# Kernel optimization log

Measured on AMD Instinct MI355X. Metric: run time of the kernel, lower is better.

## Reference

```python
import jax, jax.numpy as jnp
import numpy as np

D_MODEL = 256
D_INNER = 512   # expand=2
D_STATE = 16
D_CONV = 4
DT_RANK = 16    # ceil(d_model/16)
EPS = 1e-5


def _ln(x, g, b):
    m = x.mean(-1, keepdims=True)
    v = jnp.mean((x - m) ** 2, -1, keepdims=True)
    return (x - m) * jax.lax.rsqrt(v + EPS) * g + b


def _mamba(x, W_in, conv_w, conv_b, W_x, W_dt, b_dt, A_log, Dp, W_out):
    B, N, _ = x.shape
    xz = x @ W_in.T                               # [B,N,2*Di]
    xs, z = jnp.split(xz, 2, axis=-1)
    # depthwise causal conv1d, kernel D_CONV, left pad D_CONV-1
    xp = jnp.pad(xs, ((0, 0), (D_CONV - 1, 0), (0, 0)))
    xc = sum(xp[:, k:k + N, :] * conv_w[:, k] for k in range(D_CONV)) + conv_b
    xc = jax.nn.silu(xc)                          # [B,N,Di]
    dbl = xc @ W_x.T                              # [B,N,dt_rank+2*S]
    dt, Bm, Cm = jnp.split(dbl, [DT_RANK, DT_RANK + D_STATE], axis=-1)
    dt = jax.nn.softplus(dt @ W_dt.T + b_dt)      # [B,N,Di]
    A = -jnp.exp(A_log)                           # [Di,S]
    dA = jnp.exp(dt[..., None] * A)               # [B,N,Di,S]
    dBx = dt[..., None] * Bm[:, :, None, :] * xc[..., None]

    def step(h, inp):
        dA_t, dBx_t, c_t = inp                    # [B,Di,S],[B,Di,S],[B,S]
        h = dA_t * h + dBx_t
        y = jnp.einsum('bds,bs->bd', h, c_t)
        return h, y

    h0 = jnp.zeros((B, D_INNER, D_STATE), xs.dtype)
    _, ys = jax.lax.scan(step, h0, (dA.swapaxes(0, 1), dBx.swapaxes(0, 1), Cm.swapaxes(0, 1)))
    y = ys.swapaxes(0, 1) + Dp * xc
    y = y * jax.nn.silu(z)
    return y @ W_out.T                            # [B,N,d_model]


def setup_inputs() -> dict:
    key = jax.random.key(0)
    ks = jax.random.split(key, 24)
    g = lambda k, s, sc=0.02: jax.random.normal(k, s, jnp.float32) * sc
    inp = {}
    inp['input_states'] = jax.random.normal(ks[0], (1, 8192, D_MODEL), jnp.float32)
    inp['position_states'] = jax.random.normal(ks[1], (1, 8192, D_MODEL), jnp.float32)
    inp['W_in'] = g(ks[2], (2 * D_INNER, D_MODEL))
    inp['conv_w'] = g(ks[3], (D_INNER, D_CONV), 0.2)
    inp['conv_b'] = jnp.zeros((D_INNER,), jnp.float32)
    inp['W_x'] = g(ks[4], (DT_RANK + 2 * D_STATE, D_INNER))
    inp['W_dt'] = g(ks[5], (D_INNER, DT_RANK), 0.1)
    inp['b_dt'] = g(ks[6], (D_INNER,), 0.1)
    # S4D-real init: A_log = log(1..d_state) broadcast over channels
    inp['A_log'] = jnp.log(jnp.broadcast_to(jnp.arange(1, D_STATE + 1, dtype=jnp.float32), (D_INNER, D_STATE)))
    inp['Dp'] = jnp.ones((D_INNER,), jnp.float32)
    inp['W_out'] = g(ks[7], (D_MODEL, D_INNER))
    inp['W_lin'] = g(ks[8], (D_MODEL, D_MODEL))
    inp['b_lin'] = jnp.zeros((D_MODEL,), jnp.float32)
    inp['ln1_g'] = jnp.ones((D_MODEL,), jnp.float32)
    inp['ln1_b'] = jnp.zeros((D_MODEL,), jnp.float32)
    inp['W_exp'] = g(ks[9], (2 * D_MODEL, D_MODEL))
    inp['b_exp'] = jnp.zeros((2 * D_MODEL,), jnp.float32)
    inp['W_sq'] = g(ks[10], (D_MODEL, 2 * D_MODEL))
    inp['b_sq'] = jnp.zeros((D_MODEL,), jnp.float32)
    inp['ln2_g'] = jnp.ones((D_MODEL,), jnp.float32)
    inp['ln2_b'] = jnp.zeros((D_MODEL,), jnp.float32)
    return inp


def reference(input_states, position_states, W_in, conv_w, conv_b, W_x, W_dt, b_dt,
              A_log, Dp, W_out, W_lin, b_lin, ln1_g, ln1_b, W_exp, b_exp, W_sq, b_sq,
              ln2_g, ln2_b):
    h = _mamba(input_states, W_in, conv_w, conv_b, W_x, W_dt, b_dt, A_log, Dp, W_out)
    h = h @ W_lin.T + b_lin
    h = _ln(h + input_states, ln1_g, ln1_b)
    ff = jax.nn.relu(h @ W_exp.T + b_exp) @ W_sq.T + b_sq
    out = _ln(h + ff, ln2_g, ln2_b)
    # RPEMamba returns (hidden, input_states) as (states, attention_scores)
    return out, input_states
```

## Files before the change

kernel.cpp:

```cpp
#include <hip/hip_runtime.h>
#include <stdint.h>

#define NT 8192
#define DM 256
#define DI 512
#define DS 16
#define DR 16
#define NCH 512
#define LCH 16
#define NSUP 32
#define CPS 16

typedef __bf16 bf16_t;
typedef bf16_t bf16x8 __attribute__((ext_vector_type(8)));
typedef float f32x4 __attribute__((ext_vector_type(4)));

__device__ __forceinline__ unsigned short f2b(float f) {
    union { float f; unsigned int i; } v; v.f = f;
    unsigned int r = v.i + 0x7fffu + ((v.i >> 16) & 1u);
    return (unsigned short)(r >> 16);
}
__device__ __forceinline__ float b2f(unsigned short u) {
    union { unsigned int i; float f; } v; v.i = ((unsigned int)u) << 16; return v.f;
}
__device__ __forceinline__ bf16x8 ld_frag_lds(const unsigned short* p) {
    union { uint4 u; bf16x8 b; } v;
    v.u = *(const uint4*)p;
    return v.b;
}
__device__ __forceinline__ void async16(const unsigned short* g, unsigned short* l) {
    __builtin_amdgcn_global_load_lds(
        (const __attribute__((address_space(1))) unsigned int*)g,
        (__attribute__((address_space(3))) unsigned int*)l, 16, 0, 0);
}
__device__ __forceinline__ float fast_softplus(float x) {
    return x > 20.f ? x : __logf(1.f + __expf(x));
}
__device__ __forceinline__ float silu(float x) {
    return x / (1.f + __expf(-x));
}

struct PrepArgs {
    const float* src[6];
    unsigned short* dst[6];
    int cnt[6];
    int cvt_blocks;
    const float* W_dt;
    const float* W_x;
    unsigned short* wbig;
};
__global__ __launch_bounds__(256) void prep(PrepArgs a) {
    int blk = blockIdx.x;
    if (blk < a.cvt_blocks) {
        int i = blk * 256 + threadIdx.x;
        #pragma unroll
        for (int s = 0; s < 6; s++) {
            if (i < a.cnt[s]) {
                unsigned short v = f2b(a.src[s][i]);
                if (s == 2) {
                    int k = i >> 9, j = i & 511;
                    a.dst[s][j * 256 + k] = v;
                } else {
                    a.dst[s][i] = v;
                }
                return;
            }
            i -= a.cnt[s];
        }
    } else if (blk < a.cvt_blocks + 1024) {
        int i = (blk - a.cvt_blocks) * 256 + threadIdx.x;
        int d = i >> 9, k = i & 511;
        float acc = 0.f;
        #pragma unroll
        for (int j = 0; j < 16; j++) acc += a.W_dt[d * 16 + j] * a.W_x[j * 512 + k];
        a.wbig[d * 512 + k] = f2b(acc);
    } else {
        int i = (blk - a.cvt_blocks - 1024) * 256 + threadIdx.x;
        int j = i >> 9, k = i & 511;
        a.wbig[(512 + j) * 512 + k] = f2b(a.W_x[(16 + j) * 512 + k]);
    }
}

template<int BM, int BN, int FLAGS>
__global__ __launch_bounds__(256) void gemm_lds(
    const unsigned short* __restrict__ A, const unsigned short* __restrict__ B,
    int M, int N, int K,
    const float* __restrict__ bias, const float* __restrict__ resid,
    float* __restrict__ Cf, unsigned short* __restrict__ Cb,
    float* __restrict__ Cf2)
{
    constexpr int MI = BM / 32;
    constexpr int NJ = BN / 32;
    __shared__ unsigned short sA[BM * 64];
    __shared__ unsigned short sB[BN * 64];
    const int tid = threadIdx.x;
    const int m0 = blockIdx.x * BM;
    const int n0 = blockIdx.y * BN;
    const int wave = tid >> 6, lane = tid & 63;
    const int wm = (wave & 1) * (BM / 2);
    const int wn = (wave >> 1) * (BN / 2);
    const int qm = lane >> 4, rm = lane & 15;

    f32x4 acc[MI][NJ];
    #pragma unroll
    for (int i = 0; i < MI; i++)
        #pragma unroll
        for (int j = 0; j < NJ; j++)
            #pragma unroll
            for (int r = 0; r < 4; r++) acc[i][j][r] = 0.f;

    const int sr = tid >> 3;
    const int sc = (tid & 7) * 8;

    for (int k0 = 0; k0 < K; k0 += 64) {
        __syncthreads();
        #pragma unroll
        for (int j = 0; j < BM / 32; j++) {
            int r = sr + j * 32;
            async16(A + (size_t)(m0 + r) * K + k0 + sc, &sA[r * 64 + sc]);
        }
        #pragma unroll
        for (int j = 0; j < BN / 32; j++) {
            int r = sr + j * 32;
            if (n0 + r < N)
                async16(B + (size_t)(n0 + r) * K + k0 + sc, &sB[r * 64 + sc]);
        }
        __syncthreads();
        #pragma unroll
        for (int ks = 0; ks < 64; ks += 32) {
            bf16x8 af[MI], bfr[NJ];
            #pragma unroll
            for (int i = 0; i < MI; i++)
                af[i] = ld_frag_lds(&sA[(wm + i * 16 + rm) * 64 + ks + qm * 8]);
            #pragma unroll
            for (int j = 0; j < NJ; j++)
                bfr[j] = ld_frag_lds(&sB[(wn + j * 16 + rm) * 64 + ks + qm * 8]);
            #pragma unroll
            for (int i = 0; i < MI; i++)
                #pragma unroll
                for (int j = 0; j < NJ; j++)
                    acc[i][j] = __builtin_amdgcn_mfma_f32_16x16x32_bf16(
                        af[i], bfr[j], acc[i][j], 0, 0, 0);
        }
    }

    #pragma unroll
    for (int i = 0; i < MI; i++) {
        int mrow = m0 + wm + i * 16 + qm * 4;
        #pragma unroll
        for (int j = 0; j < NJ; j++) {
            int ncol = n0 + wn + j * 16 + rm;
            if (ncol < N) {
                #pragma unroll
                for (int r = 0; r < 4; r++) {
                    float v = acc[i][j][r];
                    int mm = mrow + r;
                    if constexpr (FLAGS & 32) {
                        if (ncol < 512) {
                            v = fast_softplus(v + bias[ncol]);
                            Cf[(size_t)mm * 512 + ncol] = v;
                        } else {
                            Cf2[(size_t)mm * 32 + (ncol - 512)] = v;
                        }
                    } else {
                        if constexpr (FLAGS & 1) v += bias[ncol];
                        if constexpr (FLAGS & 4) v += resid[(size_t)mm * N + ncol];
                        if constexpr (FLAGS & 2) v = v > 0.f ? v : 0.f;
                        if constexpr (FLAGS & 8) Cf[(size_t)mm * N + ncol] = v;
                        if constexpr (FLAGS & 16) Cb[(size_t)mm * N + ncol] = f2b(v);
                    }
                }
            }
        }
    }
}

__global__ __launch_bounds__(256) void conv_silu_b(
    const unsigned short* __restrict__ xz, const float* __restrict__ cw,
    const float* __restrict__ cb, unsigned short* __restrict__ xcb)
{
    int idx = blockIdx.x * 256 + threadIdx.x;
    int d = idx & (DI - 1), t = idx >> 9;
    float v = cb[d];
    #pragma unroll
    for (int k = 0; k < 4; k++) {
        int tt = t - 3 + k;
        if (tt >= 0) v += b2f(xz[(size_t)tt * 1024 + d]) * cw[d * 4 + k];
    }
    xcb[idx] = f2b(silu(v));
}

__global__ __launch_bounds__(256) void scan1(
    const unsigned short* __restrict__ xcb, const float* __restrict__ dtf,
    const float* __restrict__ dblf, const float* __restrict__ A_log,
    unsigned short* __restrict__ Acb, unsigned short* __restrict__ Bcb)
{
    __shared__ float sBC[LCH * 32];
    const int tid = threadIdx.x;
    const int d = blockIdx.x * 128 + (tid >> 1);
    const int sd = tid & 1;
    const int c = blockIdx.y;
    const int t0 = c * LCH;
    if (tid < 128)
        ((float4*)sBC)[tid] = ((const float4*)(dblf + (size_t)t0 * 32))[tid];
    __syncthreads();
    float A2[8], h[8];
    #pragma unroll
    for (int s = 0; s < 8; s++) {
        A2[s] = -__expf(A_log[d * 16 + sd * 8 + s]) * 1.44269504f;
        h[s] = 0.f;
    }
    float sumdt = 0.f;
    #pragma unroll 4
    for (int t = 0; t < LCH; t++) {
        float dtv = dtf[(size_t)(t0 + t) * DI + d];
        float xcv = b2f(xcb[(size_t)(t0 + t) * DI + d]);
        float dtx = dtv * xcv;
        sumdt += dtv;
        const float4 b0 = *(const float4*)&sBC[t * 32 + sd * 8];
        const float4 b1 = *(const float4*)&sBC[t * 32 + sd * 8 + 4];
        float bb[8] = {b0.x, b0.y, b0.z, b0.w, b1.x, b1.y, b1.z, b1.w};
        #pragma unroll
        for (int s = 0; s < 8; s++)
            h[s] = exp2f(dtv * A2[s]) * h[s] + dtx * bb[s];
    }
    #pragma unroll
    for (int s = 0; s < 8; s++) {
        size_t off = ((size_t)c * DS + sd * 8 + s) * DI + d;
        Acb[off] = f2b(exp2f(sumdt * A2[s]));
        Bcb[off] = f2b(h[s]);
    }
}

__global__ __launch_bounds__(256) void scan2a(
    const unsigned short* __restrict__ Acb, const unsigned short* __restrict__ Bcb,
    unsigned short* __restrict__ Apb, unsigned short* __restrict__ Hlb,
    float* __restrict__ Es, float* __restrict__ Ds)
{
    int p = blockIdx.x * 256 + threadIdx.x;
    int j = blockIdx.y;
    float h = 0.f, P = 1.f;
    for (int cc = 0; cc < CPS; cc++) {
        size_t off = (size_t)(j * CPS + cc) * 8192 + p;
        Hlb[off] = f2b(h); Apb[off] = f2b(P);
        h = b2f(Acb[off]) * h + b2f(Bcb[off]);
        P *= b2f(Acb[off]);
    }
    Es[(size_t)j * 8192 + p] = h;
    Ds[(size_t)j * 8192 + p] = P;
}

__global__ __launch_bounds__(256) void scan2b(
    const float* __restrict__ Es, const float* __restrict__ Ds,
    float* __restrict__ Ss)
{
    int p = blockIdx.x * 256 + threadIdx.x;
    float S = 0.f;
    for (int j = 0; j < NSUP; j++) {
        Ss[(size_t)j * 8192 + p] = S;
        S = Ds[(size_t)j * 8192 + p] * S + Es[(size_t)j * 8192 + p];
    }
}

__global__ __launch_bounds__(256) void scan3(
    const unsigned short* __restrict__ xcb, const float* __restrict__ dtf,
    const float* __restrict__ dblf, const unsigned short* __restrict__ xzb,
    const float* __restrict__ A_log, const float* __restrict__ Dpp,
    const unsigned short* __restrict__ Apb, const unsigned short* __restrict__ Hlb,
    const float* __restrict__ Ss, unsigned short* __restrict__ ygb)
{
    __shared__ float sBC[LCH * 32];
    const int tid = threadIdx.x;
    const int d = blockIdx.x * 128 + (tid >> 1);
    const int sd = tid & 1;
    const int c = blockIdx.y;
    const int jsup = c / CPS;
    const int t0 = c * LCH;
    if (tid < 128)
        ((float4*)sBC)[tid] = ((const float4*)(dblf + (size_t)t0 * 32))[tid];
    __syncthreads();
    float A2[8], h[8];
    #pragma unroll
    for (int s = 0; s < 8; s++) {
        A2[s] = -__expf(A_log[d * 16 + sd * 8 + s]) * 1.44269504f;
        size_t off = (size_t)c * 8192 + (sd * 8 + s) * DI + d;
        h[s] = b2f(Apb[off]) * Ss[(size_t)jsup * 8192 + (sd * 8 + s) * DI + d]
             + b2f(Hlb[off]);
    }
    const float dpv = Dpp[d];
    #pragma unroll 4
    for (int t = 0; t < LCH; t++) {
        float dtv = dtf[(size_t)(t0 + t) * DI + d];
        float xcv = b2f(xcb[(size_t)(t0 + t) * DI + d]);
        float zv  = b2f(xzb[(size_t)(t0 + t) * 1024 + DI + d]);
        float dtx = dtv * xcv;
        const float4 b0 = *(const float4*)&sBC[t * 32 + sd * 8];
        const float4 b1 = *(const float4*)&sBC[t * 32 + sd * 8 + 4];
        const float4 c0 = *(const float4*)&sBC[t * 32 + 16 + sd * 8];
        const float4 c1 = *(const float4*)&sBC[t * 32 + 16 + sd * 8 + 4];
        float bb[8] = {b0.x, b0.y, b0.z, b0.w, b1.x, b1.y, b1.z, b1.w};
        float cc[8] = {c0.x, c0.y, c0.z, c0.w, c1.x, c1.y, c1.z, c1.w};
        float y = 0.f;
        #pragma unroll
        for (int s = 0; s < 8; s++) {
            h[s] = exp2f(dtv * A2[s]) * h[s] + dtx * bb[s];
            y += h[s] * cc[s];
        }
        y += __shfl_xor(y, 1, 64);
        if (!sd)
            ygb[(size_t)(t0 + t) * DI + d] = f2b((y + dpv * xcv) * silu(zv));
    }
}

__global__ __launch_bounds__(256) void lnorm(
    const float* __restrict__ X, const float* __restrict__ X2,
    const float* __restrict__ g, const float* __restrict__ b,
    float* __restrict__ outf, unsigned short* __restrict__ outb,
    const float* __restrict__ csrc, float* __restrict__ cdst)
{
    int wave = threadIdx.x >> 6, lane = threadIdx.x & 63;
    int row = blockIdx.x * 4 + wave;
    const float* x = X + (size_t)row * DM;
    float v[4];
    #pragma unroll
    for (int i = 0; i < 4; i++) {
        int col = lane + i * 64;
        v[i] = x[col];
        if (X2) v[i] += X2[(size_t)row * DM + col];
    }
    if (cdst) {
        #pragma unroll
        for (int i = 0; i < 4; i++) {
            int col = lane + i * 64;
            cdst[(size_t)row * DM + col] = csrc[(size_t)row * DM + col];
        }
    }
    float s = v[0] + v[1] + v[2] + v[3];
    float s2 = v[0]*v[0] + v[1]*v[1] + v[2]*v[2] + v[3]*v[3];
    #pragma unroll
    for (int m = 1; m < 64; m <<= 1) {
        s  += __shfl_xor(s, m, 64);
        s2 += __shfl_xor(s2, m, 64);
    }
    float mean = s * (1.f / DM);
    float var = s2 * (1.f / DM) - mean * mean;
    float inv = rsqrtf(var + 1e-5f);
    #pragma unroll
    for (int i = 0; i < 4; i++) {
        int col = lane + i * 64;
        float o = (v[i] - mean) * inv * g[col] + b[col];
        if (outf) outf[(size_t)row * DM + col] = o;
        if (outb) outb[(size_t)row * DM + col] = f2b(o);
    }
}

static constexpr size_t OFF_XZB   = 0;
static constexpr size_t OFF_XCB   = 16777216;
static constexpr size_t OFF_DTF   = 25165824;
static constexpr size_t OFF_DBLF  = 41943040;
static constexpr size_t OFF_ACB   = 42991616;
static constexpr size_t OFF_BCB   = 51380224;
static constexpr size_t OFF_APB   = 59768832;
static constexpr size_t OFF_HLB   = 68157440;
static constexpr size_t OFF_ES    = 76546048;
static constexpr size_t OFF_DS2   = 77594624;
static constexpr size_t OFF_SS    = 78643200;
static constexpr size_t OFF_YGB   = 79691776;
static constexpr size_t OFF_XB    = 88080384;
static constexpr size_t OFF_WINB  = 92274688;
static constexpr size_t OFF_WOUTT = 92798976;
static constexpr size_t OFF_WLINB = 93061120;
static constexpr size_t OFF_WEXPB = 93192192;
static constexpr size_t OFF_WSQB  = 93454336;
static constexpr size_t OFF_WCOMB = 93716480;
static constexpr size_t OFF_WBIG  = 93978624;
static constexpr size_t OFF_H2    = 94535680;
static constexpr size_t OFF_HLN   = 102924288;
static constexpr size_t OFF_HLNB  = 111312896;
static constexpr size_t OFF_FF1B  = 115507200;
static constexpr size_t OFF_FF2   = 123895808;

extern "C" void kernel_launch(void* const* d_in, const int* in_sizes, int n_in,
                              void* d_out, int out_size, void* d_ws, size_t ws_size,
                              hipStream_t stream)
{
    const float* x      = (const float*)d_in[0];
    const float* W_in   = (const float*)d_in[2];
    const float* conv_w = (const float*)d_in[3];
    const float* conv_b = (const float*)d_in[4];
    const float* W_x    = (const float*)d_in[5];
    const float* W_dt   = (const float*)d_in[6];
    const float* b_dt   = (const float*)d_in[7];
    const float* A_log  = (const float*)d_in[8];
    const float* Dp     = (const float*)d_in[9];
    const float* W_out  = (const float*)d_in[10];
    const float* W_lin  = (const float*)d_in[11];
    const float* b_lin  = (const float*)d_in[12];
    const float* ln1_g  = (const float*)d_in[13];
    const float* ln1_b  = (const float*)d_in[14];
    const float* W_exp  = (const float*)d_in[15];
    const float* b_exp  = (const float*)d_in[16];
    const float* W_sq   = (const float*)d_in[17];
    const float* b_sq   = (const float*)d_in[18];
    const float* ln2_g  = (const float*)d_in[19];
    const float* ln2_b  = (const float*)d_in[20];

    char* ws = (char*)d_ws;
    unsigned short* xzb = (unsigned short*)(ws + OFF_XZB);
    unsigned short* xcb = (unsigned short*)(ws + OFF_XCB);
    float* dtf  = (float*)(ws + OFF_DTF);
    float* dblf = (float*)(ws + OFF_DBLF);
    unsigned short* Acb = (unsigned short*)(ws + OFF_ACB);
    unsigned short* Bcb = (unsigned short*)(ws + OFF_BCB);
    unsigned short* Apb = (unsigned short*)(ws + OFF_APB);
    unsigned short* Hlb = (unsigned short*)(ws + OFF_HLB);
    float* Es   = (float*)(ws + OFF_ES);
    float* Ds   = (float*)(ws + OFF_DS2);
    float* Ss   = (float*)(ws + OFF_SS);
    unsigned short* ygb   = (unsigned short*)(ws + OFF_YGB);
    unsigned short* xb    = (unsigned short*)(ws + OFF_XB);
    unsigned short* winb  = (unsigned short*)(ws + OFF_WINB);
    unsigned short* woutT = (unsigned short*)(ws + OFF_WOUTT);
    unsigned short* wlinb = (unsigned short*)(ws + OFF_WLINB);
    unsigned short* wexpb = (unsigned short*)(ws + OFF_WEXPB);
    unsigned short* wsqb  = (unsigned short*)(ws + OFF_WSQB);
    unsigned short* wcomb = (unsigned short*)(ws + OFF_WCOMB);
    unsigned short* wbig  = (unsigned short*)(ws + OFF_WBIG);
    float* h2   = (float*)(ws + OFF_H2);
    float* hln  = (float*)(ws + OFF_HLN);
    unsigned short* hlnb  = (unsigned short*)(ws + OFF_HLNB);
    unsigned short* ff1b  = (unsigned short*)(ws + OFF_FF1B);
    float* ff2  = (float*)(ws + OFF_FF2);
    float* outp = (float*)d_out;

    PrepArgs pa;
    pa.src[0] = x;     pa.dst[0] = xb;    pa.cnt[0] = NT * DM;
    pa.src[1] = W_in;  pa.dst[1] = winb;  pa.cnt[1] = 1024 * DM;
    pa.src[2] = W_out; pa.dst[2] = woutT; pa.cnt[2] = DM * DI;
    pa.src[3] = W_lin; pa.dst[3] = wlinb; pa.cnt[3] = DM * DM;
    pa.src[4] = W_exp; pa.dst[4] = wexpb; pa.cnt[4] = DI * DM;
    pa.src[5] = W_sq;  pa.dst[5] = wsqb;  pa.cnt[5] = DM * DI;
    pa.cvt_blocks = (2097152 + 262144 + 131072 + 65536 + 131072 + 131072) / 256;
    pa.W_dt = W_dt; pa.W_x = W_x; pa.wbig = wbig;
    prep<<<pa.cvt_blocks + 1024 + 64, 256, 0, stream>>>(pa);

    gemm_lds<64,64,16><<<dim3(4, 8), 256, 0, stream>>>(wlinb, woutT, DM, DI, DM,
        nullptr, nullptr, nullptr, wcomb, nullptr);
    gemm_lds<128,128,16><<<dim3(64, 8), 256, 0, stream>>>(xb, winb, NT, 1024, DM,
        nullptr, nullptr, nullptr, xzb, nullptr);
    conv_silu_b<<<NT * DI / 256, 256, 0, stream>>>(xzb, conv_w, conv_b, xcb);
    gemm_lds<64,64,32><<<dim3(128, 9), 256, 0, stream>>>(xcb, wbig, NT, 544, DI,
        b_dt, nullptr, dtf, nullptr, dblf);
    scan1<<<dim3(4, NCH), 256, 0, stream>>>(xcb, dtf, dblf, A_log, Acb, Bcb);
    scan2a<<<dim3(32, NSUP), 256, 0, stream>>>(Acb, Bcb, Apb, Hlb, Es, Ds);
    scan2b<<<32, 256, 0, stream>>>(Es, Ds, Ss);
    scan3<<<dim3(4, NCH), 256, 0, stream>>>(xcb, dtf, dblf, xzb, A_log, Dp,
                                            Apb, Hlb, Ss, ygb);
    gemm_lds<64,64,1|4|8><<<dim3(128, 4), 256, 0, stream>>>(ygb, wcomb, NT, DM, DI,
        b_lin, x, h2, nullptr, nullptr);
    lnorm<<<NT / 4, 256, 0, stream>>>(h2, nullptr, ln1_g, ln1_b, hln, hlnb,
                                      nullptr, nullptr);
    gemm_lds<64,128,1|2|16><<<dim3(128, 4), 256, 0, stream>>>(hlnb, wexpb, NT, DI, DM,
        b_exp, nullptr, nullptr, ff1b, nullptr);
    gemm_lds<64,64,1|8><<<dim3(128, 4), 256, 0, stream>>>(ff1b, wsqb, NT, DM, DI,
        b_sq, nullptr, ff2, nullptr, nullptr);
    lnorm<<<NT / 4, 256, 0, stream>>>(hln, ff2, ln2_g, ln2_b, outp, nullptr,
                                      x, outp + (size_t)NT * DM);
}
```

Before: 279.1 us.

## Fuse LayerNorm into output GEMMs and fold W_lin·W_out into prep kernel

Adds a gemm_ln kernel in which each block computes full 256-wide rows (a 32-row tile), then applies bias, the residual add and LayerNorm in the epilogue. This replaces the two gemm+lnorm pairs and removes the fp32 h2/ff2 intermediates and their round trips through global memory. The W_lin·W_out combined-weight GEMM moves into the prep kernel as a naive fp32 dot loop, saving one launch. Risks: only 256 blocks per fused GEMM, which lowers parallelism, and a slow 256-iteration serial loop in prep for 512 blocks.

```diff
diff --git a/kernel.cpp b/kernel.cpp
--- a/kernel.cpp
+++ b/kernel.cpp
@@ -41,30 +41,24 @@
 }
 
 struct PrepArgs {
-    const float* src[6];
-    unsigned short* dst[6];
-    int cnt[6];
+    const float* src[4];
+    unsigned short* dst[4];
+    int cnt[4];
     int cvt_blocks;
     const float* W_dt;
     const float* W_x;
+    const float* W_lin;
+    const float* W_out;
     unsigned short* wbig;
+    unsigned short* wcomb;
 };
 __global__ __launch_bounds__(256) void prep(PrepArgs a) {
     int blk = blockIdx.x;
     if (blk < a.cvt_blocks) {
         int i = blk * 256 + threadIdx.x;
         #pragma unroll
-        for (int s = 0; s < 6; s++) {
-            if (i < a.cnt[s]) {
-                unsigned short v = f2b(a.src[s][i]);
-                if (s == 2) {
-                    int k = i >> 9, j = i & 511;
-                    a.dst[s][j * 256 + k] = v;
-                } else {
-                    a.dst[s][i] = v;
-                }
-                return;
-            }
+        for (int s = 0; s < 4; s++) {
+            if (i < a.cnt[s]) { a.dst[s][i] = f2b(a.src[s][i]); return; }
             i -= a.cnt[s];
         }
     } else if (blk < a.cvt_blocks + 1024) {
@@ -74,10 +68,16 @@
         #pragma unroll
         for (int j = 0; j < 16; j++) acc += a.W_dt[d * 16 + j] * a.W_x[j * 512 + k];
         a.wbig[d * 512 + k] = f2b(acc);
-    } else {
+    } else if (blk < a.cvt_blocks + 1024 + 64) {
         int i = (blk - a.cvt_blocks - 1024) * 256 + threadIdx.x;
         int j = i >> 9, k = i & 511;
         a.wbig[(512 + j) * 512 + k] = f2b(a.W_x[(16 + j) * 512 + k]);
+    } else {
+        int i = (blk - a.cvt_blocks - 1024 - 64) * 256 + threadIdx.x;
+        int r = i >> 9, j = i & 511;
+        float acc = 0.f;
+        for (int k = 0; k < 256; k++) acc += a.W_lin[r * 256 + k] * a.W_out[k * 512 + j];
+        a.wcomb[r * 512 + j] = f2b(acc);
     }
 }
 
@@ -85,7 +85,7 @@
 __global__ __launch_bounds__(256) void gemm_lds(
     const unsigned short* __restrict__ A, const unsigned short* __restrict__ B,
     int M, int N, int K,
-    const float* __restrict__ bias, const float* __restrict__ resid,
+    const float* __restrict__ bias,
     float* __restrict__ Cf, unsigned short* __restrict__ Cb,
     float* __restrict__ Cf2)
 {
@@ -164,7 +164,6 @@
                         }
                     } else {
                         if constexpr (FLAGS & 1) v += bias[ncol];
-                        if constexpr (FLAGS & 4) v += resid[(size_t)mm * N + ncol];
                         if constexpr (FLAGS & 2) v = v > 0.f ? v : 0.f;
                         if constexpr (FLAGS & 8) Cf[(size_t)mm * N + ncol] = v;
                         if constexpr (FLAGS & 16) Cb[(size_t)mm * N + ncol] = f2b(v);
@@ -173,6 +172,115 @@
             }
         }
     }
+}
+
+__global__ __launch_bounds__(256) void gemm_ln(
+    const unsigned short* __restrict__ A, const unsigned short* __restrict__ B,
+    int K,
+    const float* __restrict__ bias, const float* __restrict__ add,
+    const float* __restrict__ g, const float* __restrict__ bv,
+    float* __restrict__ outf, unsigned short* __restrict__ outb,
+    const float* __restrict__ csrc, float* __restrict__ cdst)
+{
+    __shared__ unsigned short sA[32 * 64];
+    __shared__ unsigned short sB[256 * 64];
+    __shared__ float sSum[4][32];
+    __shared__ float sSum2[4][32];
+    const int tid = threadIdx.x;
+    const int m0 = blockIdx.x * 32;
+    const int wave = tid >> 6, lane = tid & 63;
+    const int wn = wave * 64;
+    const int qm = lane >> 4, rm = lane & 15;
+
+    f32x4 acc[2][4];
+    #pragma unroll
+    for (int i = 0; i < 2; i++)
+        #pragma unroll
+        for (int j = 0; j < 4; j++)
+            #pragma unroll
+            for (int r = 0; r < 4; r++) acc[i][j][r] = 0.f;
+
+    const int sr = tid >> 3;
+    const int sc = (tid & 7) * 8;
+
+    for (int k0 = 0; k0 < K; k0 += 64) {
+        __syncthreads();
+        async16(A + (size_t)(m0 + sr) * K + k0 + sc, &sA[sr * 64 + sc]);
+        #pragma unroll
+        for (int j = 0; j < 8; j++) {
+            int r = sr + j * 32;
+            async16(B + (size_t)r * K + k0 + sc, &sB[r * 64 + sc]);
+        }
+        __syncthreads();
+        #pragma unroll
+        for (int ks = 0; ks < 64; ks += 32) {
+            bf16x8 af[2], bfr[4];
+            #pragma unroll
+            for (int i = 0; i < 2; i++)
+                af[i] = ld_frag_lds(&sA[(i * 16 + rm) * 64 + ks + qm * 8]);
+            #pragma unroll
+            for (int j = 0; j < 4; j++)
+                bfr[j] = ld_frag_lds(&sB[(wn + j * 16 + rm) * 64 + ks + qm * 8]);
+            #pragma unroll
+            for (int i = 0; i < 2; i++)
+                #pragma unroll
+                for (int j = 0; j < 4; j++)
+                    acc[i][j] = __builtin_amdgcn_mfma_f32_16x16x32_bf16(
+                        af[i], bfr[j], acc[i][j], 0, 0, 0);
+        }
+    }
+
+    float v[2][4][4];
+    #pragma unroll
+    for (int i = 0; i < 2; i++)
+        #pragma unroll
+        for (int j = 0; j < 4; j++) {
+            int col = wn + j * 16 + rm;
+            #pragma unroll
+            for (int r = 0; r < 4; r++) {
+                int row = m0 + i * 16 + qm * 4 + r;
+                v[i][j][r] = acc[i][j][r] + bias[col] + add[(size_t)row * DM + col];
+            }
+        }
+    #pragma unroll
+    for (int i = 0; i < 2; i++)
+        #pragma unroll
+        for (int r = 0; r < 4; r++) {
+            float s  = v[i][0][r] + v[i][1][r] + v[i][2][r] + v[i][3][r];
+            float s2 = v[i][0][r]*v[i][0][r] + v[i][1][r]*v[i][1][r]
+                     + v[i][2][r]*v[i][2][r] + v[i][3][r]*v[i][3][r];
+            #pragma unroll
+            for (int m = 1; m < 16; m <<= 1) {
+                s  += __shfl_xor(s, m, 64);
+                s2 += __shfl_xor(s2, m, 64);
+            }
+            if (rm == 0) {
+                int rl = i * 16 + qm * 4 + r;
+                sSum[wave][rl] = s;
+                sSum2[wave][rl] = s2;
+            }
+        }
+    __syncthreads();
+    #pragma unroll
+    for (int i = 0; i < 2; i++)
+        #pragma unroll
+        for (int r = 0; r < 4; r++) {
+            int rl = i * 16 + qm * 4 + r;
+            int row = m0 + rl;
+            float tot  = sSum[0][rl] + sSum[1][rl] + sSum[2][rl] + sSum[3][rl];
+            float tot2 = sSum2[0][rl] + sSum2[1][rl] + sSum2[2][rl] + sSum2[3][rl];
+            float mean = tot * (1.f / DM);
+            float var  = tot2 * (1.f / DM) - mean * mean;
+            float inv  = rsqrtf(var + 1e-5f);
+            #pragma unroll
+            for (int j = 0; j < 4; j++) {
+                int col = wn + j * 16 + rm;
+                float o = (v[i][j][r] - mean) * inv * g[col] + bv[col];
+                outf[(size_t)row * DM + col] = o;
+                if (outb) outb[(size_t)row * DM + col] = f2b(o);
+                if (cdst) cdst[(size_t)row * DM + col] = csrc[(size_t)row * DM + col];
+            }
+        }
 }
 
 __global__ __launch_bounds__(256) void conv_silu_b(
@@ -312,48 +420,6 @@
     }
 }
 
-__global__ __launch_bounds__(256) void lnorm(
-    const float* __restrict__ X, const float* __restrict__ X2,
-    const float* __restrict__ g, const float* __restrict__ b,
-    float* __restrict__ outf, unsigned short* __restrict__ outb,
-    const float* __restrict__ csrc, float* __restrict__ cdst)
-{
-    int wave = threadIdx.x >> 6, lane = threadIdx.x & 63;
-    int row = blockIdx.x * 4 + wave;
-    const float* x = X + (size_t)row * DM;
-    float v[4];
-    #pragma unroll
-    for (int i = 0; i < 4; i++) {
-        int col = lane + i * 64;
-        v[i] = x[col];
-        if (X2) v[i] += X2[(size_t)row * DM + col];
-    }
-    if (cdst) {
-        #pragma unroll
-        for (int i = 0; i < 4; i++) {
-            int col = lane + i * 64;
-            cdst[(size_t)row * DM + col] = csrc[(size_t)row * DM + col];
-        }
-    }
-    float s = v[0] + v[1] + v[2] + v[3];
-    float s2 = v[0]*v[0] + v[1]*v[1] + v[2]*v[2] + v[3]*v[3];
-    #pragma unroll
-    for (int m = 1; m < 64; m <<= 1) {
-        s  += __shfl_xor(s, m, 64);
-        s2 += __shfl_xor(s2, m, 64);
-    }
-    float mean = s * (1.f / DM);
-    float var = s2 * (1.f / DM) - mean * mean;
-    float inv = rsqrtf(var + 1e-5f);
-    #pragma unroll
-    for (int i = 0; i < 4; i++) {
-        int col = lane + i * 64;
-        float o = (v[i] - mean) * inv * g[col] + b[col];
-        if (outf) outf[(size_t)row * DM + col] = o;
-        if (outb) outb[(size_t)row * DM + col] = f2b(o);
-    }
-}
-
 static constexpr size_t OFF_XZB   = 0;
 static constexpr size_t OFF_XCB   = 16777216;
 static constexpr size_t OFF_DTF   = 25165824;
@@ -368,17 +434,13 @@
 static constexpr size_t OFF_YGB   = 79691776;
 static constexpr size_t OFF_XB    = 88080384;
 static constexpr size_t OFF_WINB  = 92274688;
-static constexpr size_t OFF_WOUTT = 92798976;
-static constexpr size_t OFF_WLINB = 93061120;
-static constexpr size_t OFF_WEXPB = 93192192;
-static constexpr size_t OFF_WSQB  = 93454336;
-static constexpr size_t OFF_WCOMB = 93716480;
-static constexpr size_t OFF_WBIG  = 93978624;
-static constexpr size_t OFF_H2    = 94535680;
-static constexpr size_t OFF_HLN   = 102924288;
-static constexpr size_t OFF_HLNB  = 111312896;
-static constexpr size_t OFF_FF1B  = 115507200;
-static constexpr size_t OFF_FF2   = 123895808;
+static constexpr size_t OFF_WEXPB = 92798976;
+static constexpr size_t OFF_WSQB  = 93061120;
+static constexpr size_t OFF_WCOMB = 93323264;
+static constexpr size_t OFF_WBIG  = 93585408;
+static constexpr size_t OFF_HLN   = 94142464;
+static constexpr size_t OFF_HLNB  = 102531072;
+static constexpr size_t OFF_FF1B  = 106725376;
 
 extern "C" void kernel_launch(void* const* d_in, const int* in_sizes, int n_in,
                               void* d_out, int out_size, void* d_ws, size_t ws_size,
@@ -420,50 +482,40 @@
     unsigned short* ygb   = (unsigned short*)(ws + OFF_YGB);
     unsigned short* xb    = (unsigned short*)(ws + OFF_XB);
     unsigned short* winb  = (unsigned short*)(ws + OFF_WINB);
-    unsigned short* woutT = (unsigned short*)(ws + OFF_WOUTT);
-    unsigned short* wlinb = (unsigned short*)(ws + OFF_WLINB);
     unsigned short* wexpb = (unsigned short*)(ws + OFF_WEXPB);
     unsigned short* wsqb  = (unsigned short*)(ws + OFF_WSQB);
     unsigned short* wcomb = (unsigned short*)(ws + OFF_WCOMB);
     unsigned short* wbig  = (unsigned short*)(ws + OFF_WBIG);
-    float* h2   = (float*)(ws + OFF_H2);
     float* hln  = (float*)(ws + OFF_HLN);
     unsigned short* hlnb  = (unsigned short*)(ws + OFF_HLNB);
     unsigned short* ff1b  = (unsigned short*)(ws + OFF_FF1B);
-    float* ff2  = (float*)(ws + OFF_FF2);
     float* outp = (float*)d_out;
 
     PrepArgs pa;
     pa.src[0] = x;     pa.dst[0] = xb;    pa.cnt[0] = NT * DM;
     pa.src[1] = W_in;  pa.dst[1] = winb;  pa.cnt[1] = 1024 * DM;
-    pa.src[2] = W_out; pa.dst[2] = woutT; pa.cnt[2] = DM * DI;
-    pa.src[3] = W_lin; pa.dst[3] = wlinb; pa.cnt[3] = DM * DM;
-    pa.src[4] = W_exp; pa.dst[4] = wexpb; pa.cnt[4] = DI * DM;
-    pa.src[5] = W_sq;  pa.dst[5] = wsqb;  pa.cnt[5] = DM * DI;
-    pa.cvt_blocks = (2097152 + 262144 + 131072 + 65536 + 131072 + 131072) / 256;
-    pa.W_dt = W_dt; pa.W_x = W_x; pa.wbig = wbig;
-    prep<<<pa.cvt_blocks + 1024 + 64, 256, 0, stream>>>(pa);
-
-    gemm_lds<64,64,16><<<dim3(4, 8), 256, 0, stream>>>(wlinb, woutT, DM, DI, DM,
-        nullptr, nullptr, nullptr, wcomb, nullptr);
+    pa.src[2] = W_exp; pa.dst[2] = wexpb; pa.cnt[2] = DI * DM;
+    pa.src[3] = W_sq;  pa.dst[3] = wsqb;  pa.cnt[3] = DM * DI;
+    pa.cvt_blocks = (2097152 + 262144 + 131072 + 131072) / 256;
+    pa.W_dt = W_dt; pa.W_x = W_x; pa.W_lin = W_lin; pa.W_out = W_out;
+    pa.wbig = wbig; pa.wcomb = wcomb;
+    prep<<<pa.cvt_blocks + 1024 + 64 + 512, 256, 0, stream>>>(pa);
+
     gemm_lds<128,128,16><<<dim3(64, 8), 256, 0, stream>>>(xb, winb, NT, 1024, DM,
-        nullptr, nullptr, nullptr, xzb, nullptr);
+        nullptr, nullptr, xzb, nullptr);
     conv_silu_b<<<NT * DI / 256, 256, 0, stream>>>(xzb, conv_w, conv_b, xcb);
     gemm_lds<64,64,32><<<dim3(128, 9), 256, 0, stream>>>(xcb, wbig, NT, 544, DI,
-        b_dt, nullptr, dtf, nullptr, dblf);
+        b_dt, dtf, nullptr, dblf);
     scan1<<<dim3(4, NCH), 256, 0, stream>>>(xcb, dtf, dblf, A_log, Acb, Bcb);
     scan2a<<<dim3(32, NSUP), 256, 0, stream>>>(Acb, Bcb, Apb, Hlb, Es, Ds);
     scan2b<<<32, 256, 0, stream>>>(Es, Ds, Ss);
     scan3<<<dim3(4, NCH), 256, 0, stream>>>(xcb, dtf, dblf, xzb, A_log, Dp,
                                             Apb, Hlb, Ss, ygb);
-    gemm_lds<64,64,1|4|8><<<dim3(128, 4), 256, 0, stream>>>(ygb, wcomb, NT, DM, DI,
-        b_lin, x, h2, nullptr, nullptr);
-    lnorm<<<NT / 4, 256, 0, stream>>>(h2, nullptr, ln1_g, ln1_b, hln, hlnb,
-                                      nullptr, nullptr);
+    gemm_ln<<<NT / 32, 256, 0, stream>>>(ygb, wcomb, DI, b_lin, x,
+                                         ln1_g, ln1_b, hln, hlnb, nullptr, nullptr);
     gemm_lds<64,128,1|2|16><<<dim3(128, 4), 256, 0, stream>>>(hlnb, wexpb, NT, DI, DM,
-        b_exp, nullptr, nullptr, ff1b, nullptr);
-    gemm_lds<64,64,1|8><<<dim3(128, 4), 256, 0, stream>>>(ff1b, wsqb, NT, DM, DI,
-        b_sq, nullptr, ff2, nullptr, nullptr);
-    lnorm<<<NT / 4, 256, 0, stream>>>(hln, ff2, ln2_g, ln2_b, outp, nullptr,
-                                      x, outp + (size_t)NT * DM);
-}
+        b_exp, nullptr, ff1b, nullptr);
+    gemm_ln<<<NT / 32, 256, 0, stream>>>(ff1b, wsqb, DI, b_sq, hln,
+                                         ln2_g, ln2_b, outp, nullptr,
+                                         x, outp + (size_t)NT * DM);
+}
```

Measured after the change: 294.2 us. 1.05x slower.

## Store dt in bf16, split scan state across 4 lanes, fold W_lin*W_out into prep

Applied to the files above, without the earlier changes.

The dt projection output is now written as bf16 instead of fp32, which halves the traffic that scan1 and scan3 spend reading it. The scan kernels now give each channel 4 lanes with 4 states each instead of 2 lanes with 8, doubling the grid for more parallelism and fewer registers per thread. The combined W_lin·W_out weight is now computed directly in the prep kernel with a naive fp32 loop, removing two conversions and a separate GEMM launch. The risks are lower precision in dt and an extra shuffle stage for the y reduction.

```diff
diff --git a/kernel.cpp b/kernel.cpp
--- a/kernel.cpp
+++ b/kernel.cpp
@@ -41,30 +41,24 @@
 }
 
 struct PrepArgs {
-    const float* src[6];
-    unsigned short* dst[6];
-    int cnt[6];
+    const float* src[4];
+    unsigned short* dst[4];
+    int cnt[4];
     int cvt_blocks;
     const float* W_dt;
     const float* W_x;
+    const float* W_lin;
+    const float* W_out;
     unsigned short* wbig;
+    unsigned short* wcomb;
 };
 __global__ __launch_bounds__(256) void prep(PrepArgs a) {
     int blk = blockIdx.x;
     if (blk < a.cvt_blocks) {
         int i = blk * 256 + threadIdx.x;
         #pragma unroll
-        for (int s = 0; s < 6; s++) {
-            if (i < a.cnt[s]) {
-                unsigned short v = f2b(a.src[s][i]);
-                if (s == 2) {
-                    int k = i >> 9, j = i & 511;
-                    a.dst[s][j * 256 + k] = v;
-                } else {
-                    a.dst[s][i] = v;
-                }
-                return;
-            }
+        for (int s = 0; s < 4; s++) {
+            if (i < a.cnt[s]) { a.dst[s][i] = f2b(a.src[s][i]); return; }
             i -= a.cnt[s];
         }
     } else if (blk < a.cvt_blocks + 1024) {
@@ -74,10 +68,16 @@
         #pragma unroll
         for (int j = 0; j < 16; j++) acc += a.W_dt[d * 16 + j] * a.W_x[j * 512 + k];
         a.wbig[d * 512 + k] = f2b(acc);
-    } else {
+    } else if (blk < a.cvt_blocks + 1024 + 64) {
         int i = (blk - a.cvt_blocks - 1024) * 256 + threadIdx.x;
         int j = i >> 9, k = i & 511;
         a.wbig[(512 + j) * 512 + k] = f2b(a.W_x[(16 + j) * 512 + k]);
+    } else {
+        int i = (blk - a.cvt_blocks - 1024 - 64) * 256 + threadIdx.x;
+        int r = i >> 9, j = i & 511;
+        float acc = 0.f;
+        for (int k = 0; k < 256; k++) acc += a.W_lin[r * 256 + k] * a.W_out[k * 512 + j];
+        a.wcomb[r * 512 + j] = f2b(acc);
     }
 }
 
@@ -158,7 +158,7 @@
                     if constexpr (FLAGS & 32) {
                         if (ncol < 512) {
                             v = fast_softplus(v + bias[ncol]);
-                            Cf[(size_t)mm * 512 + ncol] = v;
+                            Cb[(size_t)mm * 512 + ncol] = f2b(v);
                         } else {
                             Cf2[(size_t)mm * 32 + (ncol - 512)] = v;
                         }
@@ -191,42 +191,41 @@
 }
 
 __global__ __launch_bounds__(256) void scan1(
-    const unsigned short* __restrict__ xcb, const float* __restrict__ dtf,
+    const unsigned short* __restrict__ xcb, const unsigned short* __restrict__ dtb,
     const float* __restrict__ dblf, const float* __restrict__ A_log,
     unsigned short* __restrict__ Acb, unsigned short* __restrict__ Bcb)
 {
     __shared__ float sBC[LCH * 32];
     const int tid = threadIdx.x;
-    const int d = blockIdx.x * 128 + (tid >> 1);
-    const int sd = tid & 1;
+    const int d = blockIdx.x * 64 + (tid >> 2);
+    const int sd = tid & 3;
     const int c = blockIdx.y;
     const int t0 = c * LCH;
     if (tid < 128)
         ((float4*)sBC)[tid] = ((const float4*)(dblf + (size_t)t0 * 32))[tid];
     __syncthreads();
-    float A2[8], h[8];
-    #pragma unroll
-    for (int s = 0; s < 8; s++) {
-        A2[s] = -__expf(A_log[d * 16 + sd * 8 + s]) * 1.44269504f;
+    float A2[4], h[4];
+    #pragma unroll
+    for (int s = 0; s < 4; s++) {
+        A2[s] = -__expf(A_log[d * 16 + sd * 4 + s]) * 1.44269504f;
         h[s] = 0.f;
     }
     float sumdt = 0.f;
     #pragma unroll 4
     for (int t = 0; t < LCH; t++) {
-        float dtv = dtf[(size_t)(t0 + t) * DI + d];
+        float dtv = b2f(dtb[(size_t)(t0 + t) * DI + d]);
         float xcv = b2f(xcb[(size_t)(t0 + t) * DI + d]);
         float dtx = dtv * xcv;
         sumdt += dtv;
-        const float4 b0 = *(const float4*)&sBC[t * 32 + sd * 8];
-        const float4 b1 = *(const float4*)&sBC[t * 32 + sd * 8 + 4];
-        float bb[8] = {b0.x, b0.y, b0.z, b0.w, b1.x, b1.y, b1.z, b1.w};
-        #pragma unroll
-        for (int s = 0; s < 8; s++)
+        const float4 b0 = *(const float4*)&sBC[t * 32 + sd * 4];
+        float bb[4] = {b0.x, b0.y, b0.z, b0.w};
+        #pragma unroll
+        for (int s = 0; s < 4; s++)
             h[s] = exp2f(dtv * A2[s]) * h[s] + dtx * bb[s];
     }
     #pragma unroll
-    for (int s = 0; s < 8; s++) {
-        size_t off = ((size_t)c * DS + sd * 8 + s) * DI + d;
+    for (int s = 0; s < 4; s++) {
+        size_t off = ((size_t)c * DS + sd * 4 + s) * DI + d;
         Acb[off] = f2b(exp2f(sumdt * A2[s]));
         Bcb[off] = f2b(h[s]);
     }
@@ -263,7 +262,7 @@
 }
 
 __global__ __launch_bounds__(256) void scan3(
-    const unsigned short* __restrict__ xcb, const float* __restrict__ dtf,
+    const unsigned short* __restrict__ xcb, const unsigned short* __restrict__ dtb,
     const float* __restrict__ dblf, const unsigned short* __restrict__ xzb,
     const float* __restrict__ A_log, const float* __restrict__ Dpp,
     const unsigned short* __restrict__ Apb, const unsigned short* __restrict__ Hlb,
@@ -271,43 +270,42 @@
 {
     __shared__ float sBC[LCH * 32];
     const int tid = threadIdx.x;
-    const int d = blockIdx.x * 128 + (tid >> 1);
-    const int sd = tid & 1;
+    const int d = blockIdx.x * 64 + (tid >> 2);
+    const int sd = tid & 3;
     const int c = blockIdx.y;
     const int jsup = c / CPS;
     const int t0 = c * LCH;
     if (tid < 128)
         ((float4*)sBC)[tid] = ((const float4*)(dblf + (size_t)t0 * 32))[tid];
     __syncthreads();
-    float A2[8], h[8];
-    #pragma unroll
-    for (int s = 0; s < 8; s++) {
-        A2[s] = -__expf(A_log[d * 16 + sd * 8 + s]) * 1.44269504f;
-        size_t off = (size_t)c * 8192 + (sd * 8 + s) * DI + d;
-        h[s] = b2f(Apb[off]) * Ss[(size_t)jsup * 8192 + (sd * 8 + s) * DI + d]
+    float A2[4], h[4];
+    #pragma unroll
+    for (int s = 0; s < 4; s++) {
+        A2[s] = -__expf(A_log[d * 16 + sd * 4 + s]) * 1.44269504f;
+        size_t off = (size_t)c * 8192 + (sd * 4 + s) * DI + d;
+        h[s] = b2f(Apb[off]) * Ss[(size_t)jsup * 8192 + (sd * 4 + s) * DI + d]
              + b2f(Hlb[off]);
     }
     const float dpv = Dpp[d];
     #pragma unroll 4
     for (int t = 0; t < LCH; t++) {
-        float dtv = dtf[(size_t)(t0 + t) * DI + d];
+        float dtv = b2f(dtb[(size_t)(t0 + t) * DI + d]);
         float xcv = b2f(xcb[(size_t)(t0 + t) * DI + d]);
         float zv  = b2f(xzb[(size_t)(t0 + t) * 1024 + DI + d]);
         float dtx = dtv * xcv;
-        const float4 b0 = *(const float4*)&sBC[t * 32 + sd * 8];
-        const float4 b1 = *(const float4*)&sBC[t * 32 + sd * 8 + 4];
-        const float4 c0 = *(const float4*)&sBC[t * 32 + 16 + sd * 8];
-        const float4 c1 = *(const float4*)&sBC[t * 32 + 16 + sd * 8 + 4];
-        float bb[8] = {b0.x, b0.y, b0.z, b0.w, b1.x, b1.y, b1.z, b1.w};
-        float cc[8] = {c0.x, c0.y, c0.z, c0.w, c1.x, c1.y, c1.z, c1.w};
+        const float4 b0 = *(const float4*)&sBC[t * 32 + sd * 4];
+        const float4 c0 = *(const float4*)&sBC[t * 32 + 16 + sd * 4];
+        float bb[4] = {b0.x, b0.y, b0.z, b0.w};
+        float cc[4] = {c0.x, c0.y, c0.z, c0.w};
         float y = 0.f;
         #pragma unroll
-        for (int s = 0; s < 8; s++) {
+        for (int s = 0; s < 4; s++) {
             h[s] = exp2f(dtv * A2[s]) * h[s] + dtx * bb[s];
             y += h[s] * cc[s];
         }
         y += __shfl_xor(y, 1, 64);
-        if (!sd)
+        y += __shfl_xor(y, 2, 64);
+        if (sd == 0)
             ygb[(size_t)(t0 + t) * DI + d] = f2b((y + dpv * xcv) * silu(zv));
     }
 }
@@ -356,7 +354,8 @@
 
 static constexpr size_t OFF_XZB   = 0;
 static constexpr size_t OFF_XCB   = 16777216;
-static constexpr size_t OFF_DTF   = 25165824;
+static constexpr size_t OFF_DTB   = 25165824;
+static constexpr size_t OFF_H2    = 33554432;
 static constexpr size_t OFF_DBLF  = 41943040;
 static constexpr size_t OFF_ACB   = 42991616;
 static constexpr size_t OFF_BCB   = 51380224;
@@ -368,17 +367,14 @@
 static constexpr size_t OFF_YGB   = 79691776;
 static constexpr size_t OFF_XB    = 88080384;
 static constexpr size_t OFF_WINB  = 92274688;
-static constexpr size_t OFF_WOUTT = 92798976;
-static constexpr size_t OFF_WLINB = 93061120;
-static constexpr size_t OFF_WEXPB = 93192192;
-static constexpr size_t OFF_WSQB  = 93454336;
-static constexpr size_t OFF_WCOMB = 93716480;
-static constexpr size_t OFF_WBIG  = 93978624;
-static constexpr size_t OFF_H2    = 94535680;
-static constexpr size_t OFF_HLN   = 102924288;
-static constexpr size_t OFF_HLNB  = 111312896;
-static constexpr size_t OFF_FF1B  = 115507200;
-static constexpr size_t OFF_FF2   = 123895808;
+static constexpr size_t OFF_WEXPB = 92798976;
+static constexpr size_t OFF_WSQB  = 93061120;
+static constexpr size_t OFF_WCOMB = 93323264;
+static constexpr size_t OFF_WBIG  = 93585408;
+static constexpr size_t OFF_HLN   = 94142464;
+static constexpr size_t OFF_HLNB  = 102531072;
+static constexpr size_t OFF_FF1B  = 106725376;
+static constexpr size_t OFF_FF2   = 115113984;
 
 extern "C" void kernel_launch(void* const* d_in, const int* in_sizes, int n_in,
                               void* d_out, int out_size, void* d_ws, size_t ws_size,
@@ -408,7 +404,8 @@
     char* ws = (char*)d_ws;
     unsigned short* xzb = (unsigned short*)(ws + OFF_XZB);
     unsigned short* xcb = (unsigned short*)(ws + OFF_XCB);
-    float* dtf  = (float*)(ws + OFF_DTF);
+    unsigned short* dtb = (unsigned short*)(ws + OFF_DTB);
+    float* h2   = (float*)(ws + OFF_H2);
     float* dblf = (float*)(ws + OFF_DBLF);
     unsigned short* Acb = (unsigned short*)(ws + OFF_ACB);
     unsigned short* Bcb = (unsigned short*)(ws + OFF_BCB);
@@ -420,13 +417,10 @@
     unsigned short* ygb   = (unsigned short*)(ws + OFF_YGB);
     unsigned short* xb    = (unsigned short*)(ws + OFF_XB);
     unsigned short* winb  = (unsigned short*)(ws + OFF_WINB);
-    unsigned short* woutT = (unsigned short*)(ws + OFF_WOUTT);
-    unsigned short* wlinb = (unsigned short*)(ws + OFF_WLINB);
     unsigned short* wexpb = (unsigned short*)(ws + OFF_WEXPB);
     unsigned short* wsqb  = (unsigned short*)(ws + OFF_WSQB);
     unsigned short* wcomb = (unsigned short*)(ws + OFF_WCOMB);
     unsigned short* wbig  = (unsigned short*)(ws + OFF_WBIG);
-    float* h2   = (float*)(ws + OFF_H2);
     float* hln  = (float*)(ws + OFF_HLN);
     unsigned short* hlnb  = (unsigned short*)(ws + OFF_HLNB);
     unsigned short* ff1b  = (unsigned short*)(ws + OFF_FF1B);
@@ -436,25 +430,22 @@
     PrepArgs pa;
     pa.src[0] = x;     pa.dst[0] = xb;    pa.cnt[0] = NT * DM;
     pa.src[1] = W_in;  pa.dst[1] = winb;  pa.cnt[1] = 1024 * DM;
-    pa.src[2] = W_out; pa.dst[2] = woutT; pa.cnt[2] = DM * DI;
-    pa.src[3] = W_lin; pa.dst[3] = wlinb; pa.cnt[3] = DM * DM;
-    pa.src[4] = W_exp; pa.dst[4] = wexpb; pa.cnt[4] = DI * DM;
-    pa.src[5] = W_sq;  pa.dst[5] = wsqb;  pa.cnt[5] = DM * DI;
-    pa.cvt_blocks = (2097152 + 262144 + 131072 + 65536 + 131072 + 131072) / 256;
-    pa.W_dt = W_dt; pa.W_x = W_x; pa.wbig = wbig;
-    prep<<<pa.cvt_blocks + 1024 + 64, 256, 0, stream>>>(pa);
-
-    gemm_lds<64,64,16><<<dim3(4, 8), 256, 0, stream>>>(wlinb, woutT, DM, DI, DM,
-        nullptr, nullptr, nullptr, wcomb, nullptr);
+    pa.src[2] = W_exp; pa.dst[2] = wexpb; pa.cnt[2] = DI * DM;
+    pa.src[3] = W_sq;  pa.dst[3] = wsqb;  pa.cnt[3] = DM * DI;
+    pa.cvt_blocks = (2097152 + 262144 + 131072 + 131072) / 256;
+    pa.W_dt = W_dt; pa.W_x = W_x; pa.W_lin = W_lin; pa.W_out = W_out;
+    pa.wbig = wbig; pa.wcomb = wcomb;
+    prep<<<pa.cvt_blocks + 1024 + 64 + 512, 256, 0, stream>>>(pa);
+
     gemm_lds<128,128,16><<<dim3(64, 8), 256, 0, stream>>>(xb, winb, NT, 1024, DM,
         nullptr, nullptr, nullptr, xzb, nullptr);
     conv_silu_b<<<NT * DI / 256, 256, 0, stream>>>(xzb, conv_w, conv_b, xcb);
     gemm_lds<64,64,32><<<dim3(128, 9), 256, 0, stream>>>(xcb, wbig, NT, 544, DI,
-        b_dt, nullptr, dtf, nullptr, dblf);
-    scan1<<<dim3(4, NCH), 256, 0, stream>>>(xcb, dtf, dblf, A_log, Acb, Bcb);
+        b_dt, nullptr, nullptr, dtb, dblf);
+    scan1<<<dim3(8, NCH), 256, 0, stream>>>(xcb, dtb, dblf, A_log, Acb, Bcb);
     scan2a<<<dim3(32, NSUP), 256, 0, stream>>>(Acb, Bcb, Apb, Hlb, Es, Ds);
     scan2b<<<32, 256, 0, stream>>>(Es, Ds, Ss);
-    scan3<<<dim3(4, NCH), 256, 0, stream>>>(xcb, dtf, dblf, xzb, A_log, Dp,
+    scan3<<<dim3(8, NCH), 256, 0, stream>>>(xcb, dtb, dblf, xzb, A_log, Dp,
                                             Apb, Hlb, Ss, ygb);
     gemm_lds<64,64,1|4|8><<<dim3(128, 4), 256, 0, stream>>>(ygb, wcomb, NT, DM, DI,
         b_lin, x, h2, nullptr, nullptr);
```

After: 300.9 us. 1.08x slower.
